# Optimization experiments

Measured on AMD Instinct MI355X. Metric: run time of the kernel, lower is better.

## Reference

```python
import jax, jax.numpy as jnp
import numpy as np

EPS_GN = 1e-5
DEN_MIN = 1e-4

B, C, H, W = 16, 256, 128, 128
MEM, NH = 64, 4
HD = MEM // NH
GROUPS = min(8, C // 4)


def setup_inputs() -> dict:
    key = jax.random.key(0)
    ks = jax.random.split(key, 12)
    s = 0.02
    x = jax.random.normal(ks[0], (B, C, H, W), jnp.float32)
    gn_w = jnp.ones((C,), jnp.float32)
    gn_b = jnp.zeros((C,), jnp.float32)
    Wk = jax.random.normal(ks[1], (MEM, C), jnp.float32) * s
    Wv = jax.random.normal(ks[2], (MEM, C), jnp.float32) * s
    Wq = jax.random.normal(ks[3], (MEM, C), jnp.float32) * s
    Wo = jax.random.normal(ks[4], (C, MEM), jnp.float32) * s
    bo = jnp.zeros((C,), jnp.float32)
    M0 = jax.random.normal(ks[5], (NH, HD, HD), jnp.float32) * s  # meta-learned warm start
    Z0 = jnp.ones((NH, HD), jnp.float32) * 0.1
    g1_w = jax.random.normal(ks[6], (C // 4, C), jnp.float32) * s
    g1_b = jnp.zeros((C // 4,), jnp.float32)
    g2_w = jax.random.normal(ks[7], (1, C // 4), jnp.float32) * s
    g2_b = jnp.full((1,), -2.0, jnp.float32)  # gate_bias
    return {"x": x, "gn_w": gn_w, "gn_b": gn_b, "Wk": Wk, "Wv": Wv, "Wq": Wq,
            "Wo": Wo, "bo": bo, "M0": M0, "Z0": Z0,
            "g1_w": g1_w, "g1_b": g1_b, "g2_w": g2_w, "g2_b": g2_b}


def _group_norm(x, w, b):
    b_, c, h, wd = x.shape
    xg = x.reshape(b_, GROUPS, c // GROUPS, h, wd)
    mu = jnp.mean(xg, axis=(2, 3, 4), keepdims=True)
    var = jnp.var(xg, axis=(2, 3, 4), keepdims=True)
    xn = ((xg - mu) * jax.lax.rsqrt(var + EPS_GN)).reshape(b_, c, h, wd)
    return xn * w[None, :, None, None] + b[None, :, None, None]


def _conv1x1(x, w):
    # x: (B,C,H,W), w: (O,C) -> (B,O,H,W)
    return jnp.einsum('bchw,oc->bohw', x, w)


def reference(x, gn_w, gn_b, Wk, Wv, Wq, Wo, bo, M0, Z0, g1_w, g1_b, g2_w, g2_b):
    bsz, c, h, w = x.shape
    n = h * w
    residual = x
    x_norm = _group_norm(x, gn_w, gn_b)

    k = _conv1x1(x_norm, Wk).reshape(bsz, NH, HD, n)
    v = _conv1x1(x_norm, Wv).reshape(bsz, NH, HD, n)
    q = _conv1x1(x_norm, Wq).reshape(bsz, NH, HD, n)

    phi_k = jax.nn.elu(k) + 1.0
    phi_q = jax.nn.elu(q) + 1.0

    M = jnp.einsum('bhdn,bhen->bhde', phi_k, v) + M0[None]
    Z = phi_k.sum(axis=-1) + Z0[None]
    y_num = jnp.einsum('bhde,bhdn->bhen', M, phi_q)
    y_den = jnp.einsum('bhd,bhdn->bhn', Z, phi_q)
    y_den = jnp.maximum(y_den, DEN_MIN)[:, :, None, :]
    y = (y_num / y_den).reshape(bsz, MEM, h, w)

    y = _conv1x1(y, Wo) + bo[None, :, None, None]

    # gate: global avg pool -> Linear -> GELU (exact) -> Linear -> sigmoid
    pooled = jnp.mean(x_norm, axis=(2, 3))  # (B, C)
    g = jax.nn.gelu(pooled @ g1_w.T + g1_b, approximate=False)
    gate = jax.nn.sigmoid(g @ g2_w.T + g2_b).reshape(bsz, 1, 1, 1)

    return residual + gate * y, gate
```

## Files before the change

kernel.cpp:

```cpp
#include <hip/hip_runtime.h>
#include <math.h>

typedef __attribute__((ext_vector_type(8))) short short8b;
typedef __attribute__((ext_vector_type(4))) float f32x4;

#define B_   16
#define C_   256
#define N_   16384
#define NH_  4
#define G_   8
#define CPG_ 32

#define OFF_S    0
#define OFF_T    4096
#define OFF_SUM  OFF_S
#define OFF_SQ   OFF_T
#define OFF_M    8192
#define OFF_Z    24576
#define OFF_GATE 25600
#define OFF_WKVQ 25616

static __device__ inline unsigned short bf16u(float f) {
    unsigned int u = __float_as_uint(f);
    return (unsigned short)((u + 0x7FFFu + ((u >> 16) & 1u)) >> 16);
}
static __device__ inline float ubf(unsigned short u) {
    return __uint_as_float(((unsigned int)u) << 16);
}

__global__ __launch_bounds__(256) void k_stats(const float* __restrict__ x,
                                               float* __restrict__ ws) {
    const int bc = blockIdx.x;
    const float4* p4 = (const float4*)(x + (size_t)bc * N_);
    float s = 0.f, q = 0.f;
    #pragma unroll 4
    for (int i = threadIdx.x; i < N_ / 4; i += 256) {
        float4 v = p4[i];
        s += v.x + v.y + v.z + v.w;
        q += v.x * v.x + v.y * v.y + v.z * v.z + v.w * v.w;
    }
    #pragma unroll
    for (int o = 32; o > 0; o >>= 1) {
        s += __shfl_down(s, o);
        q += __shfl_down(q, o);
    }
    __shared__ float ls[4], lq[4];
    const int wid = threadIdx.x >> 6, lane = threadIdx.x & 63;
    if (lane == 0) { ls[wid] = s; lq[wid] = q; }
    __syncthreads();
    if (threadIdx.x == 0) {
        ws[OFF_SUM + bc] = ls[0] + ls[1] + ls[2] + ls[3];
        ws[OFF_SQ  + bc] = lq[0] + lq[1] + lq[2] + lq[3];
    }
}

__global__ __launch_bounds__(256) void k_cvtw(const float* __restrict__ Wk,
        const float* __restrict__ Wv, const float* __restrict__ Wq,
        float* __restrict__ ws) {
    unsigned short* wkvq = (unsigned short*)(ws + OFF_WKVQ);
    const int r = blockIdx.x, t = threadIdx.x;
    const float* src = r < 64 ? Wk + r * C_
                     : r < 128 ? Wv + (r - 64) * C_
                     : Wq + (r - 128) * C_;
    wkvq[r * 256 + t] = bf16u(src[t]);
}

__global__ __launch_bounds__(256) void k_prep(
        const float* __restrict__ gnw, const float* __restrict__ gnb,
        const float* __restrict__ M0,  const float* __restrict__ Z0,
        const float* __restrict__ g1w, const float* __restrict__ g1b,
        const float* __restrict__ g2w, const float* __restrict__ g2b,
        float* __restrict__ ws, float* __restrict__ out_gate) {
    const int b = blockIdx.x, t = threadIdx.x;
    __shared__ float mu[G_], rs[G_];
    __shared__ float pooled[C_];
    __shared__ float hidden[64];

    if (t < G_) {
        float S = 0.f, Q = 0.f;
        for (int c = t * CPG_; c < (t + 1) * CPG_; ++c) {
            S += ws[OFF_SUM + b * C_ + c];
            Q += ws[OFF_SQ  + b * C_ + c];
        }
        const float cnt = (float)(CPG_ * N_);
        const float m = S / cnt;
        const float var = Q / cnt - m * m;
        mu[t] = m;
        rs[t] = rsqrtf(var + 1e-5f);
    }
    __syncthreads();
    {
        const int c = t;
        const int g = c / CPG_;
        const float sumc = ws[OFF_SUM + b * C_ + c];
        const float sc = rs[g] * gnw[c];
        const float tc = gnb[c] - mu[g] * sc;
        ws[OFF_S + b * C_ + c] = sc;
        ws[OFF_T + b * C_ + c] = tc;
        pooled[c] = fmaf(sumc * (1.f / (float)N_), sc, tc);
    }
    __syncthreads();
    if (t < 64) {
        float a = g1b[t];
        for (int c = 0; c < C_; ++c) a = fmaf(pooled[c], g1w[t * C_ + c], a);
        hidden[t] = 0.5f * a * (1.f + erff(a * 0.70710678118654752f));
    }
    __syncthreads();
    if (t == 0) {
        float z = g2b[0];
        for (int j = 0; j < 64; ++j) z = fmaf(hidden[j], g2w[j], z);
        const float gate = 1.f / (1.f + expf(-z));
        ws[OFF_GATE + b] = gate;
        out_gate[b] = gate;
    }
    for (int i = t; i < NH_ * 256; i += 256) ws[OFF_M + b * 1024 + i] = M0[i];
    for (int i = t; i < 64;        i += 256) ws[OFF_Z + b * 64 + i]   = Z0[i];
}

__global__ __launch_bounds__(256) void k_projmz(const float* __restrict__ x,
                                                float* __restrict__ ws) {
    __shared__ __align__(16) char lds[35072];
    char* w_s = lds;
    char* x_s = lds + 10240;
    unsigned short (*kvt)[136] = (unsigned short (*)[136])lds;
    float* z_red = (float*)(lds + 34816);

    const int b = blockIdx.y, px0 = blockIdx.x * 128;
    const int t = threadIdx.x, w = t >> 6, l = t & 63;
    const float* __restrict__ sv = ws + OFF_S + b * C_;
    const float* __restrict__ tv = ws + OFF_T + b * C_;
    const unsigned int* __restrict__ wkvq32 = (const unsigned int*)(ws + OFF_WKVQ);
    const float* __restrict__ xb = x + (size_t)b * C_ * N_ + px0;

    if (t < 64) z_red[t] = 0.f;

    f32x4 acc[2][8];
    #pragma unroll
    for (int i = 0; i < 2; ++i)
        #pragma unroll
        for (int j = 0; j < 8; ++j) acc[i][j] = (f32x4){0.f, 0.f, 0.f, 0.f};

    for (int ks = 0; ks < 8; ++ks) {
        __syncthreads();
        #pragma unroll
        for (int i = 0; i < 8; ++i) {
            const int e2 = t + 256 * i;
            const int row = e2 >> 4, kp = e2 & 15;
            *(unsigned int*)(w_s + row * 80 + kp * 4) =
                wkvq32[row * 128 + ks * 16 + kp];
        }
        {
            const int px = t & 127, half = t >> 7;
            #pragma unroll
            for (int i = 0; i < 8; ++i) {
                const int lc = half * 16 + i * 2;
                const int c = ks * 32 + lc;
                const float a0 = fmaf(xb[(size_t)c * N_ + px],       sv[c],     tv[c]);
                const float a1 = fmaf(xb[(size_t)(c + 1) * N_ + px], sv[c + 1], tv[c + 1]);
                *(unsigned int*)(x_s + px * 80 + lc * 2) =
                    ((unsigned int)bf16u(a1) << 16) | bf16u(a0);
            }
        }
        __syncthreads();
        short8b bfr[8];
        #pragma unroll
        for (int ct = 0; ct < 8; ++ct)
            bfr[ct] = *(const short8b*)(x_s + (ct * 16 + (l & 15)) * 80 + (l >> 4) * 16);
        #pragma unroll
        for (int rt = 0; rt < 2; ++rt) {
            const int row = w * 32 + rt * 16 + (l & 15);
            const short8b af = *(const short8b*)(w_s + row * 80 + (l >> 4) * 16);
            #pragma unroll
            for (int ct = 0; ct < 8; ++ct)
                acc[rt][ct] = __builtin_amdgcn_mfma_f32_16x16x32_bf16(
                                  af, bfr[ct], acc[rt][ct], 0, 0, 0);
        }
    }
    __syncthreads();

    #pragma unroll
    for (int rt = 0; rt < 2; ++rt) {
        const int base = w * 32 + rt * 16;
        const bool do_elu = base < 64;
        #pragma unroll
        for (int ct = 0; ct < 8; ++ct) {
            const int px = ct * 16 + (l & 15);
            #pragma unroll
            for (int r = 0; r < 4; ++r) {
                const int row = base + (l >> 4) * 4 + r;
                float v = acc[rt][ct][r];
                if (do_elu) v = v > 0.f ? v + 1.f : __expf(v);
                kvt[row][px] = bf16u(v);
            }
        }
    }
    __syncthreads();

    f32x4 accm = (f32x4){0.f, 0.f, 0.f, 0.f};
    #pragma unroll
    for (int kc = 0; kc < 4; ++kc) {
        const short8b af = *(const short8b*)((const char*)&kvt[w * 16 + (l & 15)][0]
                                             + kc * 64 + (l >> 4) * 16);
        const short8b bf = *(const short8b*)((const char*)&kvt[64 + w * 16 + (l & 15)][0]
                                             + kc * 64 + (l >> 4) * 16);
        accm = __builtin_amdgcn_mfma_f32_16x16x32_bf16(af, bf, accm, 0, 0, 0);
    }
    {
        const int zrow = t >> 2, zq = t & 3;
        float z = 0.f;
        #pragma unroll
        for (int j = 0; j < 16; ++j) {
            const unsigned int u = *(const unsigned int*)&kvt[zrow][zq * 32 + j * 2];
            z += ubf((unsigned short)u) + ubf((unsigned short)(u >> 16));
        }
        atomicAdd(&z_red[zrow], z);
    }
    #pragma unroll
    for (int r = 0; r < 4; ++r) {
        const int d = (l >> 4) * 4 + r, e = l & 15;
        atomicAdd(&ws[OFF_M + b * 1024 + w * 256 + d * 16 + e], accm[r]);
    }
    __syncthreads();
    if (t < 64) atomicAdd(&ws[OFF_Z + b * 64 + t], z_red[t]);
}

__global__ __launch_bounds__(256, 3) void k_out4(const float* __restrict__ x,
        const float* __restrict__ Wo, const float* __restrict__ bo,
        const float* __restrict__ ws, float* __restrict__ out) {
    __shared__ __align__(16) char lds[50176];
    char*  pq_s = lds;
    char*  breg = lds + 16384;
    float* bo_s = (float*)(lds + 49152);

    const int b = blockIdx.y, px0 = blockIdx.x * 128;
    const int t = threadIdx.x, w = t >> 6, l = t & 63;
    const float* __restrict__ sv = ws + OFF_S + b * C_;
    const float* __restrict__ tv = ws + OFF_T + b * C_;
    const unsigned short* __restrict__ wkvq16 = (const unsigned short*)(ws + OFF_WKVQ);
    const float* __restrict__ xb = x + (size_t)b * C_ * N_ + px0;

    bo_s[t] = bo[t];
    float* m_s = (float*)pq_s;
    for (int i = t; i < 1024; i += 256) m_s[i] = ws[OFF_M + b * 1024 + i];
    float zr[4];
    #pragma unroll
    for (int r = 0; r < 4; ++r)
        zr[r] = ws[OFF_Z + b * 64 + w * 16 + (l >> 4) * 4 + r];

    short8b afq[8];
    {
        const unsigned short* wq = wkvq16
            + (size_t)(128 + w * 16 + (l & 15)) * 256 + (l >> 4) * 8;
        #pragma unroll
        for (int ks = 0; ks < 8; ++ks) afq[ks] = *(const short8b*)(wq + ks * 32);
    }

    const int px_ = t & 127, half = t >> 7;
    char* xs0 = breg;
    char* xs1 = breg + 10240;
    char* xs2 = breg + 20480;

    f32x4 accq[8];
    #pragma unroll
    for (int j = 0; j < 8; ++j) accq[j] = (f32x4){0.f, 0.f, 0.f, 0.f};

    float xg[2][16];
    {
        #pragma unroll
        for (int i = 0; i < 16; ++i)
            xg[0][i] = xb[(size_t)(half * 16 + i) * N_ + px_];
        #pragma unroll
        for (int i = 0; i < 8; ++i) {
            const int c = half * 16 + 2 * i;
            const float a0 = fmaf(xg[0][2 * i],     sv[c],     tv[c]);
            const float a1 = fmaf(xg[0][2 * i + 1], sv[c + 1], tv[c + 1]);
            *(unsigned int*)(xs0 + px_ * 80 + (half * 16 + 2 * i) * 2) =
                ((unsigned int)bf16u(a1) << 16) | bf16u(a0);
        }
        #pragma unroll
        for (int i = 0; i < 16; ++i)
            xg[1][i] = xb[(size_t)(32 + half * 16 + i) * N_ + px_];
    }
    __syncthreads();
    #pragma unroll
    for (int ks = 0; ks < 8; ++ks) {
        char* xcur = (ks % 3 == 0) ? xs0 : (ks % 3 == 1) ? xs1 : xs2;
        if (ks + 2 < 8) {
            #pragma unroll
            for (int i = 0; i < 16; ++i)
                xg[ks & 1][i] = xb[(size_t)((ks + 2) * 32 + half * 16 + i) * N_ + px_];
        }
        #pragma unroll
        for (int ct = 0; ct < 8; ++ct) {
            const short8b bfr = *(const short8b*)(xcur + (ct * 16 + (l & 15)) * 80
                                                  + (l >> 4) * 16);
            accq[ct] = __builtin_amdgcn_mfma_f32_16x16x32_bf16(
                           afq[ks], bfr, accq[ct], 0, 0, 0);
        }
        if (ks + 1 < 8) {
            char* xnxt = ((ks + 1) % 3 == 0) ? xs0 : ((ks + 1) % 3 == 1) ? xs1 : xs2;
            #pragma unroll
            for (int i = 0; i < 8; ++i) {
                const int c = (ks + 1) * 32 + half * 16 + 2 * i;
                const float a0 = fmaf(xg[(ks + 1) & 1][2 * i],     sv[c],     tv[c]);
                const float a1 = fmaf(xg[(ks + 1) & 1][2 * i + 1], sv[c + 1], tv[c + 1]);
                *(unsigned int*)(xnxt + px_ * 80 + (half * 16 + 2 * i) * 2) =
                    ((unsigned int)bf16u(a1) << 16) | bf16u(a0);
            }
        }
        __syncthreads();
    }

    char* w2_s = breg;
    #pragma unroll
    for (int h = 0; h < NH_; ++h) {
        float wrow[16];
        #pragma unroll
        for (int j = 0; j < 4; ++j)
            *(float4*)&wrow[j * 4] = *(const float4*)&Wo[t * 64 + h * 16 + j * 4];
        float av[16];
        #pragma unroll
        for (int d = 0; d < 16; ++d) {
            float a = 0.f;
            #pragma unroll
            for (int e = 0; e < 16; ++e)
                a = fmaf(wrow[e], m_s[h * 256 + d * 16 + e], a);
            av[d] = a;
        }
        #pragma unroll
        for (int j = 0; j < 8; ++j) {
            const unsigned int pk = (unsigned int)bf16u(av[2 * j])
                                  | ((unsigned int)bf16u(av[2 * j + 1]) << 16);
            *(unsigned int*)(w2_s + t * 128 + ((h * 32 + j * 4) ^ ((t & 7) << 4))) = pk;
        }
    }
    __syncthreads();

    #pragma unroll
    for (int ct = 0; ct < 8; ++ct) {
        float p[4];
        #pragma unroll
        for (int r = 0; r < 4; ++r) {
            const float v = accq[ct][r];
            p[r] = v > 0.f ? v + 1.f : __expf(v);
        }
        float dp = 0.f;
        #pragma unroll
        for (int r = 0; r < 4; ++r) dp = fmaf(zr[r], p[r], dp);
        dp += __shfl_xor(dp, 16);
        dp += __shfl_xor(dp, 32);
        const float rd = 1.f / fmaxf(dp, 1e-4f);
        const int px = ct * 16 + (l & 15);
        const unsigned int lo = (unsigned int)bf16u(p[0] * rd)
                              | ((unsigned int)bf16u(p[1] * rd) << 16);
        const unsigned int hi = (unsigned int)bf16u(p[2] * rd)
                              | ((unsigned int)bf16u(p[3] * rd) << 16);
        const int off = (w * 32 + (l >> 4) * 8) ^ ((px & 7) << 4);
        *(unsigned long long*)(pq_s + px * 128 + off) =
            (unsigned long long)lo | ((unsigned long long)hi << 32);
    }
    __syncthreads();

    short8b bfr[2][8];
    #pragma unroll
    for (int ksi = 0; ksi < 2; ++ksi)
        #pragma unroll
        for (int ct = 0; ct < 8; ++ct) {
            const int px = ct * 16 + (l & 15);
            bfr[ksi][ct] = *(const short8b*)(pq_s + px * 128
                             + ((ksi * 64 + (l >> 4) * 16) ^ ((px & 7) << 4)));
        }
    const float gate = ws[OFF_GATE + b];
    const float* __restrict__ xr = x + (size_t)b * C_ * N_;
    float* __restrict__ ob = out + (size_t)b * C_ * N_;
    #pragma unroll
    for (int rt = 0; rt < 4; ++rt) {
        f32x4 acc[8];
        #pragma unroll
        for (int j = 0; j < 8; ++j) acc[j] = (f32x4){0.f, 0.f, 0.f, 0.f};
        const int row = w * 64 + rt * 16 + (l & 15);
        #pragma unroll
        for (int ksi = 0; ksi < 2; ++ksi) {
            const short8b af = *(const short8b*)(w2_s + row * 128
                                 + ((ksi * 64 + (l >> 4) * 16) ^ ((row & 7) << 4)));
            #pragma unroll
            for (int ct = 0; ct < 8; ++ct)
                acc[ct] = __builtin_amdgcn_mfma_f32_16x16x32_bf16(
                              af, bfr[ksi][ct], acc[ct], 0, 0, 0);
        }
        #pragma unroll
        for (int ct = 0; ct < 8; ++ct) {
            const int px = px0 + ct * 16 + (l & 15);
            #pragma unroll
            for (int r = 0; r < 4; ++r) {
                const int orow = w * 64 + rt * 16 + (l >> 4) * 4 + r;
                const size_t off = (size_t)orow * N_ + px;
                const float res = fmaf(gate, acc[ct][r] + bo_s[orow], xr[off]);
                __builtin_nontemporal_store(res, &ob[off]);
            }
        }
    }
}

extern "C" void kernel_launch(void* const* d_in, const int* in_sizes, int n_in,
                              void* d_out, int out_size, void* d_ws, size_t ws_size,
                              hipStream_t stream) {
    const float* x   = (const float*)d_in[0];
    const float* gnw = (const float*)d_in[1];
    const float* gnb = (const float*)d_in[2];
    const float* Wk  = (const float*)d_in[3];
    const float* Wv  = (const float*)d_in[4];
    const float* Wq  = (const float*)d_in[5];
    const float* Wo  = (const float*)d_in[6];
    const float* bo  = (const float*)d_in[7];
    const float* M0  = (const float*)d_in[8];
    const float* Z0  = (const float*)d_in[9];
    const float* g1w = (const float*)d_in[10];
    const float* g1b = (const float*)d_in[11];
    const float* g2w = (const float*)d_in[12];
    const float* g2b = (const float*)d_in[13];
    float* out = (float*)d_out;
    float* ws  = (float*)d_ws;

    hipLaunchKernelGGL(k_stats,  dim3(B_ * C_), dim3(256), 0, stream, x, ws);
    hipLaunchKernelGGL(k_cvtw,   dim3(192),     dim3(256), 0, stream, Wk, Wv, Wq, ws);
    hipLaunchKernelGGL(k_prep,   dim3(B_),      dim3(256), 0, stream,
                       gnw, gnb, M0, Z0, g1w, g1b, g2w, g2b, ws,
                       out + (size_t)B_ * C_ * N_);
    hipLaunchKernelGGL(k_projmz, dim3(N_ / 128, B_), dim3(256), 0, stream, x, ws);
    hipLaunchKernelGGL(k_out4,   dim3(N_ / 128, B_), dim3(256), 0, stream,
                       x, Wo, bo, ws, out);
}
```

Before: 349.4 us.

## Widen output kernel to 256-pixel tiles with 512 threads and double buffering

The output kernel now processes 256 pixels per block with 8 waves, two per head, each covering half of the pixels. This halves the number of blocks and halves the per-pixel cost of the Wo·M fold, since that work is shared over twice as many pixels. The x staging goes from three buffers with a two-stage prefetch to two buffers with a one-stage prefetch. B fragments for the second GEMM are read from LDS inside the loop instead of being held in registers, and the nontemporal output stores become plain stores. The cost is more LDS per block (about 73 KB), a shallower prefetch, and a changed occupancy target.

After: 302.0 us. 13.6% less time.

```diff
diff --git a/kernel.cpp b/kernel.cpp
--- a/kernel.cpp
+++ b/kernel.cpp
@@ -224,86 +224,85 @@
     if (t < 64) atomicAdd(&ws[OFF_Z + b * 64 + t], z_red[t]);
 }
 
-__global__ __launch_bounds__(256, 3) void k_out4(const float* __restrict__ x,
+__global__ __launch_bounds__(512, 4) void k_out5(const float* __restrict__ x,
         const float* __restrict__ Wo, const float* __restrict__ bo,
         const float* __restrict__ ws, float* __restrict__ out) {
-    __shared__ __align__(16) char lds[50176];
+    __shared__ __align__(16) char lds[74752];
     char*  pq_s = lds;
-    char*  breg = lds + 16384;
-    float* bo_s = (float*)(lds + 49152);
-
-    const int b = blockIdx.y, px0 = blockIdx.x * 128;
+    char*  breg = lds + 32768;
+    float* bo_s = (float*)(lds + 73728);
+
+    const int b = blockIdx.y, px0 = blockIdx.x * 256;
     const int t = threadIdx.x, w = t >> 6, l = t & 63;
+    const int h = w >> 1;
+    const int pxw = (w & 1) * 128;
     const float* __restrict__ sv = ws + OFF_S + b * C_;
     const float* __restrict__ tv = ws + OFF_T + b * C_;
     const unsigned short* __restrict__ wkvq16 = (const unsigned short*)(ws + OFF_WKVQ);
     const float* __restrict__ xb = x + (size_t)b * C_ * N_ + px0;
 
-    bo_s[t] = bo[t];
+    if (t < 256) bo_s[t] = bo[t];
     float* m_s = (float*)pq_s;
-    for (int i = t; i < 1024; i += 256) m_s[i] = ws[OFF_M + b * 1024 + i];
+    for (int i = t; i < 1024; i += 512) m_s[i] = ws[OFF_M + b * 1024 + i];
     float zr[4];
     #pragma unroll
     for (int r = 0; r < 4; ++r)
-        zr[r] = ws[OFF_Z + b * 64 + w * 16 + (l >> 4) * 4 + r];
+        zr[r] = ws[OFF_Z + b * 64 + h * 16 + (l >> 4) * 4 + r];
 
     short8b afq[8];
     {
         const unsigned short* wq = wkvq16
-            + (size_t)(128 + w * 16 + (l & 15)) * 256 + (l >> 4) * 8;
+            + (size_t)(128 + h * 16 + (l & 15)) * 256 + (l >> 4) * 8;
         #pragma unroll
         for (int ks = 0; ks < 8; ++ks) afq[ks] = *(const short8b*)(wq + ks * 32);
     }
 
-    const int px_ = t & 127, half = t >> 7;
+    const int px_ = t & 255, half = t >> 8;
     char* xs0 = breg;
-    char* xs1 = breg + 10240;
-    char* xs2 = breg + 20480;
+    char* xs1 = breg + 20480;
 
     f32x4 accq[8];
     #pragma unroll
     for (int j = 0; j < 8; ++j) accq[j] = (f32x4){0.f, 0.f, 0.f, 0.f};
 
-    float xg[2][16];
     {
+        float xf[16];
         #pragma unroll
         for (int i = 0; i < 16; ++i)
-            xg[0][i] = xb[(size_t)(half * 16 + i) * N_ + px_];
+            xf[i] = xb[(size_t)(half * 16 + i) * N_ + px_];
         #pragma unroll
         for (int i = 0; i < 8; ++i) {
             const int c = half * 16 + 2 * i;
-            const float a0 = fmaf(xg[0][2 * i],     sv[c],     tv[c]);
-            const float a1 = fmaf(xg[0][2 * i + 1], sv[c + 1], tv[c + 1]);
+            const float a0 = fmaf(xf[2 * i],     sv[c],     tv[c]);
+            const float a1 = fmaf(xf[2 * i + 1], sv[c + 1], tv[c + 1]);
             *(unsigned int*)(xs0 + px_ * 80 + (half * 16 + 2 * i) * 2) =
                 ((unsigned int)bf16u(a1) << 16) | bf16u(a0);
         }
-        #pragma unroll
-        for (int i = 0; i < 16; ++i)
-            xg[1][i] = xb[(size_t)(32 + half * 16 + i) * N_ + px_];
     }
     __syncthreads();
     #pragma unroll
     for (int ks = 0; ks < 8; ++ks) {
-        char* xcur = (ks % 3 == 0) ? xs0 : (ks % 3 == 1) ? xs1 : xs2;
-        if (ks + 2 < 8) {
+        char* xcur = (ks & 1) ? xs1 : xs0;
+        char* xnxt = (ks & 1) ? xs0 : xs1;
+        float xg[16];
+        if (ks < 7) {
             #pragma unroll
             for (int i = 0; i < 16; ++i)
-                xg[ks & 1][i] = xb[(size_t)((ks + 2) * 32 + half * 16 + i) * N_ + px_];
+                xg[i] = xb[(size_t)((ks + 1) * 32 + half * 16 + i) * N_ + px_];
         }
         #pragma unroll
         for (int ct = 0; ct < 8; ++ct) {
-            const short8b bfr = *(const short8b*)(xcur + (ct * 16 + (l & 15)) * 80
+            const short8b bfr = *(const short8b*)(xcur + (pxw + ct * 16 + (l & 15)) * 80
                                                   + (l >> 4) * 16);
             accq[ct] = __builtin_amdgcn_mfma_f32_16x16x32_bf16(
                            afq[ks], bfr, accq[ct], 0, 0, 0);
         }
-        if (ks + 1 < 8) {
-            char* xnxt = ((ks + 1) % 3 == 0) ? xs0 : ((ks + 1) % 3 == 1) ? xs1 : xs2;
+        if (ks < 7) {
             #pragma unroll
             for (int i = 0; i < 8; ++i) {
                 const int c = (ks + 1) * 32 + half * 16 + 2 * i;
-                const float a0 = fmaf(xg[(ks + 1) & 1][2 * i],     sv[c],     tv[c]);
-                const float a1 = fmaf(xg[(ks + 1) & 1][2 * i + 1], sv[c + 1], tv[c + 1]);
+                const float a0 = fmaf(xg[2 * i],     sv[c],     tv[c]);
+                const float a1 = fmaf(xg[2 * i + 1], sv[c + 1], tv[c + 1]);
                 *(unsigned int*)(xnxt + px_ * 80 + (half * 16 + 2 * i) * 2) =
                     ((unsigned int)bf16u(a1) << 16) | bf16u(a0);
             }
@@ -312,26 +311,30 @@
     }
 
     char* w2_s = breg;
-    #pragma unroll
-    for (int h = 0; h < NH_; ++h) {
-        float wrow[16];
-        #pragma unroll
-        for (int j = 0; j < 4; ++j)
-            *(float4*)&wrow[j * 4] = *(const float4*)&Wo[t * 64 + h * 16 + j * 4];
-        float av[16];
-        #pragma unroll
-        for (int d = 0; d < 16; ++d) {
-            float a = 0.f;
-            #pragma unroll
-            for (int e = 0; e < 16; ++e)
-                a = fmaf(wrow[e], m_s[h * 256 + d * 16 + e], a);
-            av[d] = a;
-        }
-        #pragma unroll
-        for (int j = 0; j < 8; ++j) {
-            const unsigned int pk = (unsigned int)bf16u(av[2 * j])
-                                  | ((unsigned int)bf16u(av[2 * j + 1]) << 16);
-            *(unsigned int*)(w2_s + t * 128 + ((h * 32 + j * 4) ^ ((t & 7) << 4))) = pk;
+    {
+        const int c = t & 255, hp = t >> 8;
+        #pragma unroll
+        for (int hh = 0; hh < 2; ++hh) {
+            const int hw = hp * 2 + hh;
+            float wrow[16];
+            #pragma unroll
+            for (int j = 0; j < 4; ++j)
+                *(float4*)&wrow[j * 4] = *(const float4*)&Wo[c * 64 + hw * 16 + j * 4];
+            float av[16];
+            #pragma unroll
+            for (int d = 0; d < 16; ++d) {
+                float a = 0.f;
+                #pragma unroll
+                for (int e = 0; e < 16; ++e)
+                    a = fmaf(wrow[e], m_s[hw * 256 + d * 16 + e], a);
+                av[d] = a;
+            }
+            #pragma unroll
+            for (int j = 0; j < 8; ++j) {
+                const unsigned int pk = (unsigned int)bf16u(av[2 * j])
+                                      | ((unsigned int)bf16u(av[2 * j + 1]) << 16);
+                *(unsigned int*)(w2_s + c * 128 + ((hw * 32 + j * 4) ^ ((c & 7) << 4))) = pk;
+            }
         }
     }
     __syncthreads();
@@ -350,53 +353,47 @@
         dp += __shfl_xor(dp, 16);
         dp += __shfl_xor(dp, 32);
         const float rd = 1.f / fmaxf(dp, 1e-4f);
-        const int px = ct * 16 + (l & 15);
+        const int px = pxw + ct * 16 + (l & 15);
         const unsigned int lo = (unsigned int)bf16u(p[0] * rd)
                               | ((unsigned int)bf16u(p[1] * rd) << 16);
         const unsigned int hi = (unsigned int)bf16u(p[2] * rd)
                               | ((unsigned int)bf16u(p[3] * rd) << 16);
-        const int off = (w * 32 + (l >> 4) * 8) ^ ((px & 7) << 4);
+        const int off = (h * 32 + (l >> 4) * 8) ^ ((px & 7) << 4);
         *(unsigned long long*)(pq_s + px * 128 + off) =
             (unsigned long long)lo | ((unsigned long long)hi << 32);
     }
     __syncthreads();
 
-    short8b bfr[2][8];
-    #pragma unroll
-    for (int ksi = 0; ksi < 2; ++ksi)
-        #pragma unroll
-        for (int ct = 0; ct < 8; ++ct) {
-            const int px = ct * 16 + (l & 15);
-            bfr[ksi][ct] = *(const short8b*)(pq_s + px * 128
-                             + ((ksi * 64 + (l >> 4) * 16) ^ ((px & 7) << 4)));
-        }
     const float gate = ws[OFF_GATE + b];
-    const float* __restrict__ xr = x + (size_t)b * C_ * N_;
-    float* __restrict__ ob = out + (size_t)b * C_ * N_;
+    const float* __restrict__ xr = x + (size_t)b * C_ * N_ + px0;
+    float* __restrict__ ob = out + (size_t)b * C_ * N_ + px0;
     #pragma unroll
     for (int rt = 0; rt < 4; ++rt) {
         f32x4 acc[8];
         #pragma unroll
         for (int j = 0; j < 8; ++j) acc[j] = (f32x4){0.f, 0.f, 0.f, 0.f};
-        const int row = w * 64 + rt * 16 + (l & 15);
+        const int row = h * 64 + rt * 16 + (l & 15);
         #pragma unroll
         for (int ksi = 0; ksi < 2; ++ksi) {
             const short8b af = *(const short8b*)(w2_s + row * 128
                                  + ((ksi * 64 + (l >> 4) * 16) ^ ((row & 7) << 4)));
             #pragma unroll
-            for (int ct = 0; ct < 8; ++ct)
+            for (int ct = 0; ct < 8; ++ct) {
+                const int px = pxw + ct * 16 + (l & 15);
+                const short8b bfr = *(const short8b*)(pq_s + px * 128
+                                 + ((ksi * 64 + (l >> 4) * 16) ^ ((px & 7) << 4)));
                 acc[ct] = __builtin_amdgcn_mfma_f32_16x16x32_bf16(
-                              af, bfr[ksi][ct], acc[ct], 0, 0, 0);
+                              af, bfr, acc[ct], 0, 0, 0);
+            }
         }
         #pragma unroll
         for (int ct = 0; ct < 8; ++ct) {
-            const int px = px0 + ct * 16 + (l & 15);
+            const int px = pxw + ct * 16 + (l & 15);
             #pragma unroll
             for (int r = 0; r < 4; ++r) {
-                const int orow = w * 64 + rt * 16 + (l >> 4) * 4 + r;
+                const int orow = h * 64 + rt * 16 + (l >> 4) * 4 + r;
                 const size_t off = (size_t)orow * N_ + px;
-                const float res = fmaf(gate, acc[ct][r] + bo_s[orow], xr[off]);
-                __builtin_nontemporal_store(res, &ob[off]);
+                ob[off] = fmaf(gate, acc[ct][r] + bo_s[orow], xr[off]);
             }
         }
     }
@@ -428,6 +425,6 @@
                        gnw, gnb, M0, Z0, g1w, g1b, g2w, g2b, ws,
                        out + (size_t)B_ * C_ * N_);
     hipLaunchKernelGGL(k_projmz, dim3(N_ / 128, B_), dim3(256), 0, stream, x, ws);
-    hipLaunchKernelGGL(k_out4,   dim3(N_ / 128, B_), dim3(256), 0, stream,
+    hipLaunchKernelGGL(k_out5,   dim3(N_ / 256, B_), dim3(512), 0, stream,
                        x, Wo, bo, ws, out);
 }
```
